# Optimization experiments

Hardware: AMD Instinct MI355X
Metric: run time of the kernel (lower is better)

Reference implementation:

```python
import jax, jax.numpy as jnp
import numpy as np

S, B, D, H, DH = 2048, 2, 1024, 16, 64


def setup_inputs() -> dict:
    key = jax.random.key(0)
    ks = jax.random.split(key, 7)
    sc = 0.02
    return {
        "x": jax.random.normal(ks[0], (S, B, D), jnp.float32),
        "pos_emb": jax.random.normal(ks[1], (S, D), jnp.float32),
        "pos_bias_u": jax.random.normal(ks[2], (H, DH), jnp.float32) * sc,
        "pos_bias_v": jax.random.normal(ks[3], (H, DH), jnp.float32) * sc,
        "W_qkv": jax.random.normal(ks[4], (D, 3 * H * DH), jnp.float32) * sc,
        "W_relemb": jax.random.normal(ks[5], (D, H * DH), jnp.float32) * sc,
        "W_o": jax.random.normal(ks[6], (H * DH, D), jnp.float32) * sc,
        "ln_gamma": jnp.ones((D,), jnp.float32),
        "ln_beta": jnp.zeros((D,), jnp.float32),
    }


def _rel_shift(x):
    # x: [i, j, b, n]; Transformer-XL relative shift
    i, j, b, n = x.shape
    zero_pad = jnp.zeros((i, 1, b, n), x.dtype)
    xp = jnp.concatenate([zero_pad, x], axis=1)      # [i, j+1, b, n]
    xp = xp.reshape(j + 1, i, b, n)
    return xp[1:].reshape(i, j, b, n)


def reference(x, pos_emb, pos_bias_u, pos_bias_v, W_qkv, W_relemb, W_o, ln_gamma, ln_beta):
    seq_len, batch, d_model = x.shape
    num_head, d_head = pos_bias_u.shape
    scale = jnp.asarray(1.0 / d_head ** 0.5, x.dtype)

    qkv = x @ W_qkv                                   # [S,B,3*H*DH]
    q, k, v = jnp.split(qkv, 3, axis=-1)
    q = q.reshape(seq_len, batch, num_head, d_head)
    k = k.reshape(seq_len, batch, num_head, d_head)
    v = v.reshape(seq_len, batch, num_head, d_head)
    r = (pos_emb @ W_relemb).reshape(seq_len, num_head, d_head)

    AC = jnp.einsum('ibnd,jbnd->ijbn', q + pos_bias_u, k)
    BD = _rel_shift(jnp.einsum('ibnd,jnd->ijbn', q + pos_bias_v, r))
    attn_score = (AC + BD) * scale                    # [S,S,B,H]
    attn_prob = jax.nn.softmax(attn_score, axis=1)

    attn_vec = jnp.einsum('ijbn,jbnd->ibnd', attn_prob, v)
    attn_vec = attn_vec.reshape(seq_len, batch, num_head * d_head)
    attn_out = attn_vec @ W_o

    y = x + attn_out
    mu = jnp.mean(y, axis=-1, keepdims=True)
    var = jnp.mean(jnp.square(y - mu), axis=-1, keepdims=True)
    y_norm = (y - mu) * jax.lax.rsqrt(var + 1e-5)
    return y_norm * ln_gamma + ln_beta
```

## Files before the change

kernel.cpp:

```cpp
#include <hip/hip_runtime.h>
#include <stdint.h>

#define S_LEN 2048
#define BATCH 2
#define DMODEL 1024
#define NHEAD 16
#define DHEAD 64
#define HS ((size_t)S_LEN * DHEAD)

typedef float floatx4 __attribute__((ext_vector_type(4)));
typedef __bf16 bf16x8 __attribute__((ext_vector_type(8)));

__device__ __forceinline__ float bf2f(uint16_t u) {
  union { uint32_t i; float f; } x; x.i = ((uint32_t)u) << 16; return x.f;
}
__device__ __forceinline__ uint16_t f2bf(float f) {
  union { float f; uint32_t i; } x; x.f = f;
  uint32_t r = x.i + 0x7fffu + ((x.i >> 16) & 1u);
  return (uint16_t)(r >> 16);
}
__device__ __forceinline__ uint16_t f2bf_hw(float f) {
  __bf16 h = (__bf16)f;
  union { __bf16 h; uint16_t u; } c; c.h = h; return c.u;
}
__device__ __forceinline__ uint4 ld8(const void* p, size_t idx, int isf32) {
  if (isf32) {
    const float* f = (const float*)p + idx;
    float4 a = *(const float4*)f;
    float4 b = *(const float4*)(f + 4);
    uint4 r; uint16_t* rp = (uint16_t*)&r;
    rp[0] = f2bf(a.x); rp[1] = f2bf(a.y); rp[2] = f2bf(a.z); rp[3] = f2bf(a.w);
    rp[4] = f2bf(b.x); rp[5] = f2bf(b.y); rp[6] = f2bf(b.z); rp[7] = f2bf(b.w);
    return r;
  }
  return *(const uint4*)((const uint16_t*)p + idx);
}
__device__ __forceinline__ float ld1(const void* p, size_t idx, int isf32) {
  return isf32 ? ((const float*)p)[idx] : bf2f(((const uint16_t*)p)[idx]);
}
__device__ __forceinline__ uint4 addb8(uint4 a, uint4 b) {
  uint4 r;
  const uint16_t* pa = (const uint16_t*)&a;
  const uint16_t* pb = (const uint16_t*)&b;
  uint16_t* pr = (uint16_t*)&r;
#pragma unroll
  for (int e = 0; e < 8; e++) pr[e] = f2bf(bf2f(pa[e]) + bf2f(pb[e]));
  return r;
}

__global__ __launch_bounds__(256) void detect_dtype(const void* __restrict__ x,
                                                    int* __restrict__ flag) {
  __shared__ int cnt;
  if (threadIdx.x == 0) cnt = 0;
  __syncthreads();
  const uint16_t w = ((const uint16_t*)x)[threadIdx.x];
  const float v = bf2f(w);
  const float av = fabsf(v);
  if (!(av <= 256.f)) atomicAdd(&cnt, 1);
  __syncthreads();
  if (threadIdx.x == 0) *flag = (cnt >= 8) ? 1 : 0;
}

__global__ __launch_bounds__(256) void cvt_x(const void* __restrict__ x,
                                             uint16_t* __restrict__ xb,
                                             const int* __restrict__ pflag) {
  const int isf32 = *pflag;
  const size_t gid = (size_t)blockIdx.x * 256 + threadIdx.x;
  const int d0 = (int)(gid & (DMODEL / 8 - 1)) * 8;
  const size_t sb = gid >> 7;
  const size_t s = sb >> 1, b = sb & 1;
  uint4 v = ld8(x, sb * DMODEL + d0, isf32);
  *(uint4*)&xb[(b * S_LEN + s) * DMODEL + d0] = v;
}

__global__ __launch_bounds__(256) void cvt_mat(const void* __restrict__ src,
                                               uint16_t* __restrict__ dst,
                                               const int* __restrict__ pflag) {
  const int isf32 = *pflag;
  const size_t gid = ((size_t)blockIdx.x * 256 + threadIdx.x) * 8;
  *(uint4*)&dst[gid] = ld8(src, gid, isf32);
}

__global__ __launch_bounds__(256) void cvt_matT(const void* __restrict__ src,
                                                uint16_t* __restrict__ dst,
                                                int R, int C,
                                                const int* __restrict__ pflag) {
  __shared__ uint16_t lT[64 * 72];
  const int isf32 = *pflag;
  const int tid = threadIdx.x;
  const int c0 = blockIdx.x * 64;
  const int r0 = blockIdx.y * 64;
  {
    const int rr = tid >> 2, cc = (tid & 3) * 16;
    *(uint4*)&lT[rr * 72 + cc]     = ld8(src, (size_t)(r0 + rr) * C + c0 + cc, isf32);
    *(uint4*)&lT[rr * 72 + cc + 8] = ld8(src, (size_t)(r0 + rr) * C + c0 + cc + 8, isf32);
  }
  __syncthreads();
  const int oc = tid >> 2, rc = (tid & 3) * 16;
  uint16_t tmp[16];
#pragma unroll
  for (int e = 0; e < 16; e++) tmp[e] = lT[(rc + e) * 72 + oc];
  uint16_t* dp = dst + (size_t)(c0 + oc) * R + r0 + rc;
  *(uint4*)dp = *(const uint4*)&tmp[0];
  *(uint4*)(dp + 8) = *(const uint4*)&tmp[8];
}

__global__ __launch_bounds__(256) void qkv_gemm(
    const uint16_t* __restrict__ xb, const uint16_t* __restrict__ peb,
    const uint16_t* __restrict__ wqT, const uint16_t* __restrict__ wrT,
    uint16_t* __restrict__ qb, uint16_t* __restrict__ kb,
    uint16_t* __restrict__ vb, uint16_t* __restrict__ rb, int z0) {
  __shared__ uint16_t lA[128 * 72];
  __shared__ uint16_t lB[128 * 72];
  const int tid = threadIdx.x;
  const int lane = tid & 63;
  const int wave = tid >> 6;
  const int wm = wave >> 1, wn = wave & 1;
  const int strip = blockIdx.x;
  const int zg0 = z0 + 2 * blockIdx.z;
  const int b = zg0 >> 4, h0 = zg0 & 15;

  const uint16_t* Ab;
  const uint16_t* BT;
  int col0;
  if (strip < 3) {
    Ab = xb + (size_t)b * S_LEN * DMODEL;
    BT = wqT; col0 = strip * DMODEL + h0 * 64;
  } else {
    Ab = peb;
    BT = wrT; col0 = h0 * 64;
  }
  Ab += (size_t)blockIdx.y * 128 * DMODEL;

  floatx4 acc[4][4];
  floatx4 zero4 = {0.f, 0.f, 0.f, 0.f};
#pragma unroll
  for (int i = 0; i < 4; i++)
#pragma unroll
    for (int j = 0; j < 4; j++) acc[i][j] = zero4;

  const int srow = tid >> 1;
  const int skc = (tid & 1) * 32;
  const int l15 = lane & 15;
  const int l4 = lane >> 4;

  for (int k0 = 0; k0 < DMODEL; k0 += 64) {
    const uint16_t* ap = Ab + (size_t)srow * DMODEL + k0 + skc;
    const uint16_t* bp = BT + (size_t)(col0 + srow) * DMODEL + k0 + skc;
#pragma unroll
    for (int e = 0; e < 4; e++) {
      *(uint4*)&lA[srow * 72 + skc + e * 8] = *(const uint4*)(ap + e * 8);
      *(uint4*)&lB[srow * 72 + skc + e * 8] = *(const uint4*)(bp + e * 8);
    }
    __syncthreads();
#pragma unroll
    for (int ks = 0; ks < 2; ks++) {
      bf16x8 af[4], bfr[4];
#pragma unroll
      for (int mi = 0; mi < 4; mi++)
        af[mi] = *(const bf16x8*)&lA[(wm * 64 + mi * 16 + l15) * 72 + ks * 32 + l4 * 8];
#pragma unroll
      for (int ni = 0; ni < 4; ni++)
        bfr[ni] = *(const bf16x8*)&lB[(wn * 64 + ni * 16 + l15) * 72 + ks * 32 + l4 * 8];
#pragma unroll
      for (int mi = 0; mi < 4; mi++)
#pragma unroll
        for (int ni = 0; ni < 4; ni++)
          acc[mi][ni] = __builtin_amdgcn_mfma_f32_16x16x32_bf16(af[mi], bfr[ni], acc[mi][ni], 0, 0, 0);
    }
    __syncthreads();
  }

  uint16_t* ob = (strip == 0) ? qb : (strip == 1) ? kb : (strip == 2) ? vb : rb;
  const int r0 = blockIdx.y * 128 + wm * 64;
  const int zlb = 2 * blockIdx.z;
#pragma unroll
  for (int mi = 0; mi < 4; mi++)
#pragma unroll
    for (int ni = 0; ni < 4; ni++)
#pragma unroll
      for (int v = 0; v < 4; v++) {
        const int sg = r0 + mi * 16 + (lane >> 4) * 4 + v;
        const int c  = wn * 64 + ni * 16 + (lane & 15);
        const int zl = zlb + (c >> 6);
        const int d  = c & 63;
        ob[(size_t)zl * HS + (size_t)sg * 64 + d] = f2bf_hw(acc[mi][ni][v]);
      }
}

__global__ __launch_bounds__(256) void transpose_v(const uint16_t* __restrict__ vb,
                                                   uint16_t* __restrict__ vt) {
  __shared__ uint16_t lT[64 * 72];
  const int tid = threadIdx.x;
  const int zl = blockIdx.y;
  const int j0 = blockIdx.x * 64;
  const uint16_t* src = vb + (size_t)zl * HS + (size_t)j0 * 64;
  {
    const int j = tid >> 2, dc = (tid & 3) * 16;
    *(uint4*)&lT[j * 72 + dc] = *(const uint4*)(src + (size_t)j * 64 + dc);
    *(uint4*)&lT[j * 72 + dc + 8] = *(const uint4*)(src + (size_t)j * 64 + dc + 8);
  }
  __syncthreads();
  const int d = tid >> 2, jc = (tid & 3) * 16;
  uint16_t tmp[16];
#pragma unroll
  for (int e = 0; e < 16; e++) tmp[e] = lT[(jc + e) * 72 + d];
  uint16_t* dst = vt + (size_t)zl * HS + (size_t)d * S_LEN + j0 + jc;
  *(uint4*)dst = *(const uint4*)&tmp[0];
  *(uint4*)(dst + 8) = *(const uint4*)&tmp[8];
}

#define FBP 72
#define VTP 136
#define PBP 136
#define SC2 0.180336880f

#define FA_ISSUE(bxn) do {                                                  \
    const uint16_t* spk_ = kz + (size_t)((bxn) * 128 + sj) * 64 + skc;      \
    kr0 = *(const uint4*)spk_;                                              \
    kr1 = *(const uint4*)(spk_ + 8);                                        \
    const uint16_t* spv_ = vz + (size_t)sd * S_LEN + (bxn) * 128 + sjc;     \
    vr0 = *(const uint4*)spv_;                                              \
    vr1 = *(const uint4*)(spv_ + 8);                                        \
    const int Dq_ = ((bxn) - by) * 128 + sslot - 127;                       \
    int rrow_ = (Dq_ <= 0) ? (Dq_ + S_LEN - 1) : (Dq_ - 2 < 0 ? 0 : Dq_ - 2); \
    if (rrow_ > S_LEN - 1) rrow_ = S_LEN - 1;                               \
    const uint16_t* spr_ = rz + (size_t)rrow_ * 64 + shalf;                 \
    br0 = *(const uint4*)spr_;                                              \
    br1 = *(const uint4*)(spr_ + 8);                                        \
    br2 = *(const uint4*)(spr_ + 16);                                       \
    br3 = *(const uint4*)(spr_ + 24);                                       \
  } while (0)

#define FA_COMMIT() do {                                                    \
    *(uint4*)&lK[sj * FBP + skc]     = kr0;                                 \
    *(uint4*)&lK[sj * FBP + skc + 8] = kr1;                                 \
    *(uint4*)&lV[sd * VTP + sjc]     = vr0;                                 \
    *(uint4*)&lV[sd * VTP + sjc + 8] = vr1;                                 \
    uint16_t* dp_ = &lR[sslot * FBP + shalf];                               \
    *(uint4*)(dp_)      = br0;                                              \
    *(uint4*)(dp_ + 8)  = br1;                                              \
    *(uint4*)(dp_ + 16) = br2;                                              \
    *(uint4*)(dp_ + 24) = br3;                                              \
  } while (0)

__global__ __launch_bounds__(512, 2) void flash_attn(
    const uint16_t* __restrict__ qb, const uint16_t* __restrict__ kb,
    const uint16_t* __restrict__ vt, const uint16_t* __restrict__ rb,
    const void* __restrict__ bu, const void* __restrict__ bv,
    uint16_t* __restrict__ avec, int z0, int zc,
    const int* __restrict__ pflag) {
  __shared__ uint16_t lK[128 * FBP];
  __shared__ uint16_t lV[64 * VTP];
  __shared__ uint16_t lR[256 * FBP];
  __shared__ uint16_t lP[8 * 16 * PBP];
  const int isf32 = *pflag;
  const int tid = threadIdx.x;
  const int lane = tid & 63;
  const int w = tid >> 6;
  const int l15 = lane & 15;
  const int l4 = lane >> 4;
  int by, zl;
  {
    const int bid = blockIdx.x;
    if ((zc & 7) == 0) {
      const int xcd = bid & 7;
      const int t = bid >> 3;
      by = t & 15;
      zl = xcd + 8 * (t >> 4);
    } else {
      by = bid & 15;
      zl = bid >> 4;
    }
  }
  const int zg = z0 + zl;
  const int b = zg >> 4, h = zg & 15;
  const int i0 = by * 128;

  const uint16_t* qz = qb + (size_t)zl * HS;
  const uint16_t* kz = kb + (size_t)zl * HS;
  const uint16_t* vz = vt + (size_t)zl * HS;
  const uint16_t* rz = rb + (size_t)zl * HS;
  uint16_t* pbw = lP + w * 16 * PBP;
  const int cmin = 112 - 16 * w;
  const int r_loc = l4 * 4;

  const int sj = tid >> 2, skc = (tid & 3) * 16;
  const int sd = tid >> 3, sjc = (tid & 7) * 16;
  const int sslot = tid >> 1, shalf = (tid & 1) * 32;

  uint4 kr0, kr1, vr0, vr1, br0, br1, br2, br3;

  uint4 af1[2], af2[2], af2s[2];
  {
    const int qrow = i0 + w * 16 + l15;
    const int qrow1 = min(qrow + 1, S_LEN - 1);
#pragma unroll
    for (int ks = 0; ks < 2; ks++) {
      const int kc = ks * 32 + l4 * 8;
      uint4 bub = ld8(bu, (size_t)h * 64 + kc, isf32);
      uint4 bvb = ld8(bv, (size_t)h * 64 + kc, isf32);
      uint4 qv  = *(const uint4*)(qz + (size_t)qrow * 64 + kc);
      uint4 qv1 = *(const uint4*)(qz + (size_t)qrow1 * 64 + kc);
      af1[ks]  = addb8(qv, bub);
      af2[ks]  = addb8(qv, bvb);
      af2s[ks] = addb8(qv1, bvb);
    }
  }

  floatx4 acc_o[4];
  floatx4 zero4 = {0.f, 0.f, 0.f, 0.f};
#pragma unroll
  for (int i = 0; i < 4; i++) acc_o[i] = zero4;
  float m[4] = {-1e30f, -1e30f, -1e30f, -1e30f};
  float l[4] = {0.f, 0.f, 0.f, 0.f};

  FA_ISSUE(0);
  FA_COMMIT();
  __syncthreads();

  for (int bx = 0; bx < 16; ++bx) {
    const int del = bx - by;
    if (bx < 15) FA_ISSUE(bx + 1);

    floatx4 accp[9];
#pragma unroll
    for (int f = 0; f < 9; f++) accp[f] = zero4;
#pragma unroll
    for (int ks = 0; ks < 2; ks++) {
      const bf16x8 a1 = *(const bf16x8*)&af2[ks];
      const bf16x8 a2 = *(const bf16x8*)&af2s[ks];
#pragma unroll
      for (int f = 0; f < 9; f++) {
        const int cb = cmin + 16 * f;
        const bf16x8 brg = *(const bf16x8*)&lR[(cb + l15) * FBP + ks * 32 + l4 * 8];
        const bf16x8 a = (cb >= 128 - 128 * del) ? a2 : a1;
        accp[f] = __builtin_amdgcn_mfma_f32_16x16x32_bf16(a, brg, accp[f], 0, 0, 0);
      }
    }
    floatx4 acc_s[8];
#pragma unroll
    for (int f = 0; f < 8; f++) acc_s[f] = zero4;
#pragma unroll
    for (int ks = 0; ks < 2; ks++) {
      const bf16x8 a = *(const bf16x8*)&af1[ks];
#pragma unroll
      for (int f = 0; f < 8; f++) {
        const bf16x8 bk = *(const bf16x8*)&lK[(f * 16 + l15) * FBP + ks * 32 + l4 * 8];
        acc_s[f] = __builtin_amdgcn_mfma_f32_16x16x32_bf16(a, bk, acc_s[f], 0, 0, 0);
      }
    }

    float rmax[4] = {-1e30f, -1e30f, -1e30f, -1e30f};
#pragma unroll
    for (int v = 0; v < 4; v++) {
      const int r = r_loc + v;
      const int srcl = l4 * 16 + ((l15 + 15 - r) & 15);
      float sh[9];
#pragma unroll
      for (int f = 0; f < 9; f++) sh[f] = __shfl(accp[f][v], srcl);
      const int Dbase = del * 128 + l15 - w * 16 - r;
#pragma unroll
      for (int f = 0; f < 8; f++) {
        float bd = (l15 <= r) ? sh[f] : sh[f + 1];
        if (Dbase + 16 * f == 1) bd = 0.f;
        const float sv = (acc_s[f][v] + bd) * SC2;
        acc_s[f][v] = sv;
        rmax[v] = fmaxf(rmax[v], sv);
      }
    }
#pragma unroll
    for (int v = 0; v < 4; v++) {
#pragma unroll
      for (int o = 1; o < 16; o <<= 1) rmax[v] = fmaxf(rmax[v], __shfl_xor(rmax[v], o));
      const float mn = fmaxf(m[v], rmax[v]);
      const float al = __builtin_amdgcn_exp2f(m[v] - mn);
      m[v] = mn;
      l[v] *= al;
#pragma unroll
      for (int nd = 0; nd < 4; nd++) acc_o[nd][v] *= al;
    }
    float rsum[4] = {0.f, 0.f, 0.f, 0.f};
#pragma unroll
    for (int f = 0; f < 8; f++)
#pragma unroll
      for (int v = 0; v < 4; v++) {
        const float p = __builtin_amdgcn_exp2f(acc_s[f][v] - m[v]);
        acc_s[f][v] = p;
        rsum[v] += p;
      }
#pragma unroll
    for (int v = 0; v < 4; v++) {
#pragma unroll
      for (int o = 1; o < 16; o <<= 1) rsum[v] += __shfl_xor(rsum[v], o);
      l[v] += rsum[v];
    }
#pragma unroll
    for (int f = 0; f < 8; f++)
#pragma unroll
      for (int v = 0; v < 4; v++)
        pbw[(r_loc + v) * PBP + f * 16 + l15] = f2bf_hw(acc_s[f][v]);

#pragma unroll
    for (int ks = 0; ks < 4; ks++) {
      const bf16x8 ap = *(const bf16x8*)&pbw[l15 * PBP + ks * 32 + l4 * 8];
#pragma unroll
      for (int nd = 0; nd < 4; nd++) {
        const bf16x8 bvv = *(const bf16x8*)&lV[(nd * 16 + l15) * VTP + ks * 32 + l4 * 8];
        acc_o[nd] = __builtin_amdgcn_mfma_f32_16x16x32_bf16(ap, bvv, acc_o[nd], 0, 0, 0);
      }
    }

    __syncthreads();
    if (bx < 15) {
      FA_COMMIT();
      __syncthreads();
    }
  }

#pragma unroll
  for (int v = 0; v < 4; v++) {
    const float inv = 1.f / l[v];
    const int i = i0 + w * 16 + r_loc + v;
#pragma unroll
    for (int nd = 0; nd < 4; nd++) {
      const int d = nd * 16 + l15;
      avec[((size_t)i * BATCH + b) * DMODEL + h * 64 + d] = f2bf_hw(acc_o[nd][v] * inv);
    }
  }
}

__global__ __launch_bounds__(256) void out_gemm(
    const uint16_t* __restrict__ avec, const uint16_t* __restrict__ woT,
    const void* __restrict__ x, uint16_t* __restrict__ ybuf,
    const int* __restrict__ pflag) {
  __shared__ uint16_t lA[128 * 72];
  __shared__ uint16_t lB[128 * 72];
  const int isf32 = *pflag;
  const int tid = threadIdx.x;
  const int lane = tid & 63;
  const int wave = tid >> 6;
  const int wm = wave >> 1, wn = wave & 1;
  const uint16_t* Ab = avec + (size_t)blockIdx.y * 128 * DMODEL;
  const int col0 = blockIdx.x * 128;

  floatx4 acc[4][4];
  floatx4 zero4 = {0.f, 0.f, 0.f, 0.f};
#pragma unroll
  for (int i = 0; i < 4; i++)
#pragma unroll
    for (int j = 0; j < 4; j++) acc[i][j] = zero4;

  const int srow = tid >> 1;
  const int skc = (tid & 1) * 32;
  const int l15 = lane & 15;
  const int l4 = lane >> 4;

  for (int k0 = 0; k0 < DMODEL; k0 += 64) {
    const uint16_t* ap = Ab + (size_t)srow * DMODEL + k0 + skc;
    const uint16_t* bp = woT + (size_t)(col0 + srow) * DMODEL + k0 + skc;
#pragma unroll
    for (int e = 0; e < 4; e++) {
      *(uint4*)&lA[srow * 72 + skc + e * 8] = *(const uint4*)(ap + e * 8);
      *(uint4*)&lB[srow * 72 + skc + e * 8] = *(const uint4*)(bp + e * 8);
    }
    __syncthreads();
#pragma unroll
    for (int ks = 0; ks < 2; ks++) {
      bf16x8 af[4], bfr[4];
#pragma unroll
      for (int mi = 0; mi < 4; mi++)
        af[mi] = *(const bf16x8*)&lA[(wm * 64 + mi * 16 + l15) * 72 + ks * 32 + l4 * 8];
#pragma unroll
      for (int ni = 0; ni < 4; ni++)
        bfr[ni] = *(const bf16x8*)&lB[(wn * 64 + ni * 16 + l15) * 72 + ks * 32 + l4 * 8];
#pragma unroll
      for (int mi = 0; mi < 4; mi++)
#pragma unroll
        for (int ni = 0; ni < 4; ni++)
          acc[mi][ni] = __builtin_amdgcn_mfma_f32_16x16x32_bf16(af[mi], bfr[ni], acc[mi][ni], 0, 0, 0);
    }
    __syncthreads();
  }

  const int r0 = blockIdx.y * 128 + wm * 64;
#pragma unroll
  for (int mi = 0; mi < 4; mi++)
#pragma unroll
    for (int ni = 0; ni < 4; ni++)
#pragma unroll
      for (int v = 0; v < 4; v++) {
        const int rg = r0 + mi * 16 + (lane >> 4) * 4 + v;
        const int cg = col0 + wn * 64 + ni * 16 + (lane & 15);
        const size_t o = (size_t)rg * DMODEL + cg;
        ybuf[o] = f2bf_hw(acc[mi][ni][v] + ld1(x, o, isf32));
      }
}

__global__ __launch_bounds__(256) void ln_f32(
    const uint16_t* __restrict__ y, const void* __restrict__ gamma,
    const void* __restrict__ beta, float* __restrict__ out,
    const int* __restrict__ pflag) {
  const int isf32 = *pflag;
  const int row = blockIdx.x;
  const int tid = threadIdx.x;
  const int lane = tid & 63, wave = tid >> 6;
  const uint16_t* yr = y + (size_t)row * DMODEL;
  uint2 u = *(const uint2*)(yr + tid * 4);
  const uint16_t* up = (const uint16_t*)&u;
  float f[4];
  float s = 0.f, q = 0.f;
#pragma unroll
  for (int j = 0; j < 4; j++) { f[j] = bf2f(up[j]); s += f[j]; q += f[j] * f[j]; }
#pragma unroll
  for (int o = 32; o; o >>= 1) { s += __shfl_xor(s, o); q += __shfl_xor(q, o); }
  __shared__ float rs[4], rq[4];
  if (lane == 0) { rs[wave] = s; rq[wave] = q; }
  __syncthreads();
  s = rs[0] + rs[1] + rs[2] + rs[3];
  q = rq[0] + rq[1] + rq[2] + rq[3];
  const float mu = s * (1.f / DMODEL);
  const float var = fmaxf(q * (1.f / DMODEL) - mu * mu, 0.f);
  const float inv = rsqrtf(var + 1e-5f);
  float4 o4;
  float* op = (float*)&o4;
#pragma unroll
  for (int j = 0; j < 4; j++) {
    const int c = tid * 4 + j;
    float r = (f[j] - mu) * inv * ld1(gamma, c, isf32) + ld1(beta, c, isf32);
    if (!(r == r)) r = 1e4f;
    op[j] = r;
  }
  *(float4*)(out + (size_t)row * DMODEL + tid * 4) = o4;
}

__global__ __launch_bounds__(256) void sentinel_fill(float* __restrict__ out) {
  const size_t i = (size_t)blockIdx.x * 1024 + threadIdx.x * 4;
  out[i] = 1e6f; out[i + 1] = 1e6f; out[i + 2] = 1e6f; out[i + 3] = 1e6f;
}

extern "C" void kernel_launch(void* const* d_in, const int* in_sizes, int n_in,
                              void* d_out, int out_size, void* d_ws, size_t ws_size,
                              hipStream_t stream) {
  const void* x    = d_in[0];
  const void* pe   = d_in[1];
  const void* bu   = d_in[2];
  const void* bv   = d_in[3];
  const void* Wqkv = d_in[4];
  const void* Wrel = d_in[5];
  const void* Wo   = d_in[6];
  const void* gam  = d_in[7];
  const void* bet  = d_in[8];
  float* out = (float*)d_out;

  const size_t per_z = 5 * HS * 2;
  const size_t conv_bytes = (size_t)(8 + 4 + 6 + 2 + 2) * 1024 * 1024;
  int ZC = 0;
  for (int c = 32; c >= 2; c >>= 1)
    if (256 + (size_t)c * per_z + conv_bytes <= ws_size) { ZC = c; break; }

  const dim3 blk(256);
  if (ZC == 0) {
    sentinel_fill<<<dim3(4096), blk, 0, stream>>>(out);
    return;
  }

  int* flag = (int*)d_ws;
  uint16_t* qb  = (uint16_t*)((char*)d_ws + 256);
  uint16_t* kb  = qb + (size_t)ZC * HS;
  uint16_t* vb  = kb + (size_t)ZC * HS;
  uint16_t* rb  = vb + (size_t)ZC * HS;
  uint16_t* vtb = rb + (size_t)ZC * HS;
  uint16_t* xbuf = vtb + (size_t)ZC * HS;
  uint16_t* peb  = xbuf + (size_t)BATCH * S_LEN * DMODEL;
  uint16_t* wqT  = peb + (size_t)S_LEN * DMODEL;
  uint16_t* wrT  = wqT + (size_t)DMODEL * 3 * DMODEL;
  uint16_t* woT  = wrT + (size_t)DMODEL * DMODEL;
  uint16_t* ybuf = xbuf;
  uint16_t* avec = (uint16_t*)d_out;

  detect_dtype<<<dim3(1), blk, 0, stream>>>(x, flag);
  cvt_x<<<dim3(2048), blk, 0, stream>>>(x, xbuf, flag);
  cvt_mat<<<dim3(1024), blk, 0, stream>>>(pe, peb, flag);
  cvt_matT<<<dim3(48, 16), blk, 0, stream>>>(Wqkv, wqT, DMODEL, 3 * DMODEL, flag);
  cvt_matT<<<dim3(16, 16), blk, 0, stream>>>(Wrel, wrT, DMODEL, DMODEL, flag);
  cvt_matT<<<dim3(16, 16), blk, 0, stream>>>(Wo,   woT, DMODEL, DMODEL, flag);

  for (int z0 = 0; z0 < 32; z0 += ZC) {
    qkv_gemm<<<dim3(4, 16, ZC / 2), blk, 0, stream>>>(xbuf, peb, wqT, wrT,
                                                      qb, kb, vb, rb, z0);
    transpose_v<<<dim3(32, ZC), blk, 0, stream>>>(vb, vtb);
    flash_attn<<<dim3(16 * ZC), dim3(512), 0, stream>>>(qb, kb, vtb, rb, bu, bv,
                                                        avec, z0, ZC, flag);
  }

  out_gemm<<<dim3(8, 32, 1), blk, 0, stream>>>(avec, woT, x, ybuf, flag);
  ln_f32<<<dim3(4096), blk, 0, stream>>>(ybuf, gam, bet, out, flag);
}
```

Before: 361.3 us.

## Dedup R projection across batches, XCD-aware QKV grid, lazy softmax rescale

The QKV GEMM moves to a 1D grid whose block index is decoded so that neighbouring work lands on the same XCD. When all 32 batch-head slices are processed in one pass, the blocks that would recompute the pos_emb projection for the second batch exit early, and flash attention reads the shared R buffer through the head index. The flash kernel splits the rel-shift pass into a masked path for diagonal tiles and an unmasked path for the rest. It also skips the online-softmax rescale unless the row max grows by more than 8 (log2 units), which saves exp and multiply work but lets exponentials grow up to 2^8 before renormalisation.

Measured after the change: 368.8 us. 1.02x slower.

```diff
diff --git a/kernel.cpp b/kernel.cpp
--- a/kernel.cpp
+++ b/kernel.cpp
@@ -109,16 +109,23 @@
     const uint16_t* __restrict__ xb, const uint16_t* __restrict__ peb,
     const uint16_t* __restrict__ wqT, const uint16_t* __restrict__ wrT,
     uint16_t* __restrict__ qb, uint16_t* __restrict__ kb,
-    uint16_t* __restrict__ vb, uint16_t* __restrict__ rb, int z0) {
+    uint16_t* __restrict__ vb, uint16_t* __restrict__ rb, int z0, int dedup) {
   __shared__ uint16_t lA[128 * 72];
   __shared__ uint16_t lB[128 * 72];
   const int tid = threadIdx.x;
   const int lane = tid & 63;
   const int wave = tid >> 6;
   const int wm = wave >> 1, wn = wave & 1;
-  const int strip = blockIdx.x;
-  const int zg0 = z0 + 2 * blockIdx.z;
+  const int bid = blockIdx.x;
+  const int xcd = bid & 7;
+  const int rem = bid >> 3;
+  const int strip = rem & 3;
+  const int gy = xcd + 8 * (rem >> 2);
+  const int by = gy & 15;
+  const int t  = gy >> 4;
+  const int zg0 = z0 + 2 * t;
   const int b = zg0 >> 4, h0 = zg0 & 15;
+  if (strip == 3 && dedup && (zg0 & 16)) return;
 
   const uint16_t* Ab;
   const uint16_t* BT;
@@ -130,7 +137,7 @@
     Ab = peb;
     BT = wrT; col0 = h0 * 64;
   }
-  Ab += (size_t)blockIdx.y * 128 * DMODEL;
+  Ab += (size_t)by * 128 * DMODEL;
 
   floatx4 acc[4][4];
   floatx4 zero4 = {0.f, 0.f, 0.f, 0.f};
@@ -172,8 +179,8 @@
   }
 
   uint16_t* ob = (strip == 0) ? qb : (strip == 1) ? kb : (strip == 2) ? vb : rb;
-  const int r0 = blockIdx.y * 128 + wm * 64;
-  const int zlb = 2 * blockIdx.z;
+  const int r0 = by * 128 + wm * 64;
+  const int zlb = 2 * t;
 #pragma unroll
   for (int mi = 0; mi < 4; mi++)
 #pragma unroll
@@ -214,6 +221,7 @@
 #define VTP 136
 #define PBP 136
 #define SC2 0.180336880f
+#define DTHR 8.0f
 
 #define FA_ISSUE(bxn) do {                                                  \
     const uint16_t* spk_ = kz + (size_t)((bxn) * 128 + sj) * 64 + skc;      \
@@ -280,7 +288,7 @@
   const uint16_t* qz = qb + (size_t)zl * HS;
   const uint16_t* kz = kb + (size_t)zl * HS;
   const uint16_t* vz = vt + (size_t)zl * HS;
-  const uint16_t* rz = rb + (size_t)zl * HS;
+  const uint16_t* rz = rb + (size_t)(zc >= 16 ? (zg & 15) : zl) * HS;
   uint16_t* pbw = lP + w * 16 * PBP;
   const int cmin = 112 - 16 * w;
   const int r_loc = l4 * 4;
@@ -352,33 +360,52 @@
     }
 
     float rmax[4] = {-1e30f, -1e30f, -1e30f, -1e30f};
+    if (del == 0 || del == 1) {
+#pragma unroll
+      for (int v = 0; v < 4; v++) {
+        const int r = r_loc + v;
+        const int srcl = l4 * 16 + ((l15 + 15 - r) & 15);
+        float sh[9];
+#pragma unroll
+        for (int f = 0; f < 9; f++) sh[f] = __shfl(accp[f][v], srcl);
+        const int Dbase = del * 128 + l15 - w * 16 - r;
+#pragma unroll
+        for (int f = 0; f < 8; f++) {
+          float bd = (l15 <= r) ? sh[f] : sh[f + 1];
+          if (Dbase + 16 * f == 1) bd = 0.f;
+          const float sv = (acc_s[f][v] + bd) * SC2;
+          acc_s[f][v] = sv;
+          rmax[v] = fmaxf(rmax[v], sv);
+        }
+      }
+    } else {
+#pragma unroll
+      for (int v = 0; v < 4; v++) {
+        const int r = r_loc + v;
+        const int srcl = l4 * 16 + ((l15 + 15 - r) & 15);
+        float sh[9];
+#pragma unroll
+        for (int f = 0; f < 9; f++) sh[f] = __shfl(accp[f][v], srcl);
+#pragma unroll
+        for (int f = 0; f < 8; f++) {
+          const float bd = (l15 <= r) ? sh[f] : sh[f + 1];
+          const float sv = (acc_s[f][v] + bd) * SC2;
+          acc_s[f][v] = sv;
+          rmax[v] = fmaxf(rmax[v], sv);
+        }
+      }
+    }
 #pragma unroll
     for (int v = 0; v < 4; v++) {
-      const int r = r_loc + v;
-      const int srcl = l4 * 16 + ((l15 + 15 - r) & 15);
-      float sh[9];
-#pragma unroll
-      for (int f = 0; f < 9; f++) sh[f] = __shfl(accp[f][v], srcl);
-      const int Dbase = del * 128 + l15 - w * 16 - r;
-#pragma unroll
-      for (int f = 0; f < 8; f++) {
-        float bd = (l15 <= r) ? sh[f] : sh[f + 1];
-        if (Dbase + 16 * f == 1) bd = 0.f;
-        const float sv = (acc_s[f][v] + bd) * SC2;
-        acc_s[f][v] = sv;
-        rmax[v] = fmaxf(rmax[v], sv);
-      }
-    }
-#pragma unroll
-    for (int v = 0; v < 4; v++) {
 #pragma unroll
       for (int o = 1; o < 16; o <<= 1) rmax[v] = fmaxf(rmax[v], __shfl_xor(rmax[v], o));
-      const float mn = fmaxf(m[v], rmax[v]);
-      const float al = __builtin_amdgcn_exp2f(m[v] - mn);
-      m[v] = mn;
-      l[v] *= al;
-#pragma unroll
-      for (int nd = 0; nd < 4; nd++) acc_o[nd][v] *= al;
+      if (rmax[v] > m[v] + DTHR) {
+        const float al = __builtin_amdgcn_exp2f(m[v] - rmax[v]);
+        m[v] = rmax[v];
+        l[v] *= al;
+#pragma unroll
+        for (int nd = 0; nd < 4; nd++) acc_o[nd][v] *= al;
+      }
     }
     float rsum[4] = {0.f, 0.f, 0.f, 0.f};
 #pragma unroll
@@ -564,6 +591,7 @@
     sentinel_fill<<<dim3(4096), blk, 0, stream>>>(out);
     return;
   }
+  const int dedup = (ZC >= 16) ? 1 : 0;
 
   int* flag = (int*)d_ws;
   uint16_t* qb  = (uint16_t*)((char*)d_ws + 256);
@@ -587,8 +615,8 @@
   cvt_matT<<<dim3(16, 16), blk, 0, stream>>>(Wo,   woT, DMODEL, DMODEL, flag);
 
   for (int z0 = 0; z0 < 32; z0 += ZC) {
-    qkv_gemm<<<dim3(4, 16, ZC / 2), blk, 0, stream>>>(xbuf, peb, wqT, wrT,
-                                                      qb, kb, vb, rb, z0);
+    qkv_gemm<<<dim3(4 * 16 * (ZC / 2)), blk, 0, stream>>>(xbuf, peb, wqT, wrT,
+                                                          qb, kb, vb, rb, z0, dedup);
     transpose_v<<<dim3(32, ZC), blk, 0, stream>>>(vb, vtb);
     flash_attn<<<dim3(16 * ZC), dim3(512), 0, stream>>>(qb, kb, vtb, rb, bu, bv,
                                                         avec, z0, ZC, flag);
```
